# Kernel optimization log

Measured on AMD Instinct MI355X. Metric: run time of the kernel, lower is better.

Reference implementation:

```python
import jax, jax.numpy as jnp
import numpy as np

N = 100000      # nodes
E = 1600000     # edges (avg degree 16)
K = 3           # num_stacks
T = 4           # num_layers
H = 16          # hidden channels (conv1 out)
C = 1           # num_classes
BN_EPS = 1e-5


def setup_inputs() -> dict:
    key = jax.random.key(0)
    ks = jax.random.split(key, 14)
    s = 0.1
    return {
        "x": jax.random.normal(ks[0], (N, 1), jnp.float32),
        "edge_index": jax.random.randint(ks[1], (2, E), 0, N, dtype=jnp.int64),
        "edge_weight": jax.random.uniform(ks[2], (E,), jnp.float32),
        # conv1 (ARMAConv 1->16, K stacks, shared weights)
        "w1_init": jax.random.normal(ks[3], (K, 1, H), jnp.float32) * s,
        "w1_w":    jax.random.normal(ks[4], (K, H, H), jnp.float32) * s,
        "w1_root": jax.random.normal(ks[5], (K, 1, H), jnp.float32) * s,
        "w1_b":    jax.random.normal(ks[6], (K, H), jnp.float32) * s,
        "bn1_g": jnp.ones((H,), jnp.float32),
        "bn1_b": jnp.zeros((H,), jnp.float32),
        # conv2 (ARMAConv 16->1, act=None)
        "w2_init": jax.random.normal(ks[7], (K, H, C), jnp.float32) * s,
        "w2_w":    jax.random.normal(ks[8], (K, C, C), jnp.float32) * s,
        "w2_root": jax.random.normal(ks[9], (K, H, C), jnp.float32) * s,
        "w2_b":    jax.random.normal(ks[10], (K, C), jnp.float32) * s,
        # end linear 1->1
        "lin_w": jax.random.normal(ks[11], (C, C), jnp.float32) * s,
        "lin_b": jnp.zeros((C,), jnp.float32),
    }


def _arma_conv(x, src, dst, norm, init_w, w, root_w, bias, act):
    """PyG ARMAConv with shared weights. x: [N,Fin] -> [N,Fout]."""
    n = x.shape[0]
    # root/skip term (dropout is identity in eval); bias broadcast per stack
    root = jnp.einsum('ni,kio->nko', x, root_w) + bias[None, :, :]  # [N,K,Fout]
    out = jnp.einsum('ni,kio->nko', x, init_w)                      # t=0 transform
    for t in range(T):
        if t > 0:
            out = jnp.einsum('nki,kio->nko', out, w)                # shared weight
        msg = out[src] * norm[:, None, None]                        # [E,K,Fout]
        out = jax.ops.segment_sum(msg, dst, num_segments=n)         # A_hat @ out
        out = out + root
        if act:
            out = jax.nn.relu(out)
    return out.mean(axis=1)  # average over stacks


def reference(x, edge_index, edge_weight, w1_init, w1_w, w1_root, w1_b,
              bn1_g, bn1_b, w2_init, w2_w, w2_root, w2_b, lin_w, lin_b):
    src, dst = edge_index[0], edge_index[1]
    n = x.shape[0]
    # gcn_norm without self loops
    deg = jax.ops.segment_sum(edge_weight, dst, num_segments=n)
    dis = jnp.where(deg > 0, 1.0 / jnp.sqrt(deg), 0.0)
    norm = dis[src] * edge_weight * dis[dst]

    h = _arma_conv(x, src, dst, norm, w1_init, w1_w, w1_root, w1_b, act=True)
    # BatchNorm1d over node dim (batch statistics, deterministic)
    mu = h.mean(axis=0)
    var = h.var(axis=0)
    h = (h - mu) / jnp.sqrt(var + BN_EPS) * bn1_g + bn1_b
    h = jax.nn.relu(h)
    # dropout is identity in eval
    h = _arma_conv(h, src, dst, norm, w2_init, w2_w, w2_root, w2_b, act=False)
    h = h @ lin_w.T + lin_b
    return jax.nn.sigmoid(h)
```

## Files before the change

### kernel.cpp

```cpp
#include <hip/hip_runtime.h>
#include <hip/hip_bf16.h>
#include <math.h>


__global__ void zero_kernel(float* p, int n) {
    int i = blockIdx.x * blockDim.x + threadIdx.x;
    if (i < n) p[i] = 0.f;
}

__global__ void rank_kernel(const int* __restrict__ ei, int* __restrict__ cnt,
                            int* __restrict__ rank, int E) {
    int i = blockIdx.x * blockDim.x + threadIdx.x;
    if (i >= E) return;
    int dst = ei[E + i];
    rank[i] = atomicAdd(&cnt[dst], 1);
}

__global__ void scan1(const int* cnt, int* row_ptr, int* blockSums, int n) {
    __shared__ int sh[1024];
    int i = blockIdx.x * 1024 + threadIdx.x;
    int v = (i < n) ? cnt[i] : 0;
    sh[threadIdx.x] = v;
    __syncthreads();
    for (int off = 1; off < 1024; off <<= 1) {
        int t = 0;
        if (threadIdx.x >= off) t = sh[threadIdx.x - off];
        __syncthreads();
        sh[threadIdx.x] += t;
        __syncthreads();
    }
    if (i < n) row_ptr[i] = sh[threadIdx.x] - v;
    if (threadIdx.x == 1023) blockSums[blockIdx.x] = sh[1023];
}

__global__ void scan2(int* blockSums, int nb) {
    if (threadIdx.x == 0 && blockIdx.x == 0) {
        int run = 0;
        for (int i = 0; i < nb; i++) { int v = blockSums[i]; blockSums[i] = run; run += v; }
    }
}

__global__ void scan3(int* row_ptr, const int* blockSums, int n, int E) {
    int i = blockIdx.x * 1024 + threadIdx.x;
    if (i < n) row_ptr[i] += blockSums[blockIdx.x];
    if (i == 0) row_ptr[n] = E;
}

__global__ void place2(const int* __restrict__ ei, const float* __restrict__ ew,
                       const int* __restrict__ rank, const int* __restrict__ row_ptr,
                       int2* __restrict__ csr, int E) {
    int i = blockIdx.x * blockDim.x + threadIdx.x;
    if (i >= E) return;
    int s = ei[i];
    int d = ei[E + i];
    int pos = row_ptr[d] + rank[i];
    csr[pos] = make_int2(s, __float_as_int(ew[i]));
}

__global__ void wdeg_dis(const int2* __restrict__ csr, const int* __restrict__ row_ptr,
                         float* __restrict__ dis, int n) {
    int node = blockIdx.x * blockDim.x + threadIdx.x;
    if (node >= n) return;
    int p = row_ptr[node], end = row_ptr[node + 1];
    float s = 0.f;
    for (; p < end; p++) s += __int_as_float(csr[p].y);
    dis[node] = (s > 0.f) ? (1.0f / sqrtf(s)) : 0.f;
}

__global__ void normk(int2* __restrict__ csr, const int* __restrict__ row_ptr,
                      const float* __restrict__ dis, int n) {
    int node = blockIdx.x * blockDim.x + threadIdx.x;
    if (node >= n) return;
    int p = row_ptr[node], end = row_ptr[node + 1];
    float dn = dis[node];
    for (; p < end; p++) {
        int2 e = csr[p];
        csr[p].y = __float_as_int(__int_as_float(e.y) * dn * dis[e.x]);
    }
}


__global__ void aggx(const float* __restrict__ x, const int* __restrict__ row_ptr,
                     const int2* __restrict__ csr, float* __restrict__ y, int n) {
    int node = blockIdx.x * blockDim.x + threadIdx.x;
    if (node >= n) return;
    int p = row_ptr[node], end = row_ptr[node + 1];
    float a0 = 0.f, a1 = 0.f, a2 = 0.f, a3 = 0.f, a4 = 0.f, a5 = 0.f, a6 = 0.f, a7 = 0.f;
    for (; p + 7 < end; p += 8) {
        int2 e0 = csr[p], e1 = csr[p+1], e2 = csr[p+2], e3 = csr[p+3];
        int2 e4 = csr[p+4], e5 = csr[p+5], e6 = csr[p+6], e7 = csr[p+7];
        a0 += x[e0.x] * __int_as_float(e0.y);
        a1 += x[e1.x] * __int_as_float(e1.y);
        a2 += x[e2.x] * __int_as_float(e2.y);
        a3 += x[e3.x] * __int_as_float(e3.y);
        a4 += x[e4.x] * __int_as_float(e4.y);
        a5 += x[e5.x] * __int_as_float(e5.y);
        a6 += x[e6.x] * __int_as_float(e6.y);
        a7 += x[e7.x] * __int_as_float(e7.y);
    }
    for (; p + 1 < end; p += 2) {
        int2 e0 = csr[p], e1 = csr[p+1];
        a0 += x[e0.x] * __int_as_float(e0.y);
        a1 += x[e1.x] * __int_as_float(e1.y);
    }
    if (p < end) { int2 e = csr[p]; a0 += x[e.x] * __int_as_float(e.y); }
    y[node] = ((a0 + a1) + (a2 + a3)) + ((a4 + a5) + (a6 + a7));
}

__global__ void init48(const float* __restrict__ x, const float* __restrict__ y,
                       const float* __restrict__ w_init, const float* __restrict__ w_root,
                       const float* __restrict__ w_b, __hip_bfloat16* __restrict__ P, int n) {
    unsigned t = blockIdx.x * blockDim.x + threadIdx.x;
    if (t >= (unsigned)n * 64u) return;
    unsigned node = t >> 6, c = t & 63;
    float v = 0.f;
    if (c < 48) v = fmaxf(y[node] * w_init[c] + x[node] * w_root[c] + w_b[c], 0.f);
    P[t] = __float2bfloat16(v);
}

__global__ void __launch_bounds__(256) agg48f(
    const __hip_bfloat16* __restrict__ P, const float* __restrict__ W,
    const float* __restrict__ x, const float* __restrict__ w_root,
    const float* __restrict__ w_b, const int* __restrict__ row_ptr,
    const int2* __restrict__ csr, __hip_bfloat16* __restrict__ Pout, int n) {
    int wid = (int)((blockIdx.x * blockDim.x + threadIdx.x) >> 6);
    int lane = threadIdx.x & 63;
    if (wid >= n) return;
    unsigned orow = (unsigned)wid * 64u;
    if (lane >= 48) { Pout[orow + lane] = __float2bfloat16(0.f); return; }
    int k = lane >> 4, o = lane & 15;
    float wv[16];
#pragma unroll
    for (int i = 0; i < 16; i++) wv[i] = W[k * 256 + i * 16 + o];

    int p = row_ptr[wid], end = row_ptr[wid + 1];
    float a0 = 0.f, a1 = 0.f, a2 = 0.f, a3 = 0.f, a4 = 0.f, a5 = 0.f, a6 = 0.f, a7 = 0.f;
    for (; p + 7 < end; p += 8) {
        int2 e0 = csr[p], e1 = csr[p+1], e2 = csr[p+2], e3 = csr[p+3];
        int2 e4 = csr[p+4], e5 = csr[p+5], e6 = csr[p+6], e7 = csr[p+7];
        float q0 = __bfloat162float(P[(unsigned)e0.x * 64u + lane]);
        float q1 = __bfloat162float(P[(unsigned)e1.x * 64u + lane]);
        float q2 = __bfloat162float(P[(unsigned)e2.x * 64u + lane]);
        float q3 = __bfloat162float(P[(unsigned)e3.x * 64u + lane]);
        float q4 = __bfloat162float(P[(unsigned)e4.x * 64u + lane]);
        float q5 = __bfloat162float(P[(unsigned)e5.x * 64u + lane]);
        float q6 = __bfloat162float(P[(unsigned)e6.x * 64u + lane]);
        float q7 = __bfloat162float(P[(unsigned)e7.x * 64u + lane]);
        a0 += q0 * __int_as_float(e0.y);
        a1 += q1 * __int_as_float(e1.y);
        a2 += q2 * __int_as_float(e2.y);
        a3 += q3 * __int_as_float(e3.y);
        a4 += q4 * __int_as_float(e4.y);
        a5 += q5 * __int_as_float(e5.y);
        a6 += q6 * __int_as_float(e6.y);
        a7 += q7 * __int_as_float(e7.y);
    }
    for (; p + 1 < end; p += 2) {
        int2 e0 = csr[p], e1 = csr[p+1];
        a0 += __bfloat162float(P[(unsigned)e0.x * 64u + lane]) * __int_as_float(e0.y);
        a1 += __bfloat162float(P[(unsigned)e1.x * 64u + lane]) * __int_as_float(e1.y);
    }
    if (p < end) {
        int2 e = csr[p];
        a0 += __bfloat162float(P[(unsigned)e.x * 64u + lane]) * __int_as_float(e.y);
    }
    float S = ((a0 + a1) + (a2 + a3)) + ((a4 + a5) + (a6 + a7));

    float acc = 0.f;
    int base = lane & 48;
#pragma unroll
    for (int i = 0; i < 16; i++) {
        float sv = __shfl(S, base + i, 64);
        acc += sv * wv[i];
    }
    float v = acc + x[wid] * w_root[lane] + w_b[lane];
    Pout[orow + lane] = __float2bfloat16(fmaxf(v, 0.f));
}


__global__ void bn_stats(const __hip_bfloat16* __restrict__ P, float* __restrict__ acc, int n) {
    int tid = threadIdx.x;
    int c = tid & 15;
    int rowSlot = (int)((blockIdx.x * blockDim.x + tid) >> 4);
    int rowStride = (int)((gridDim.x * blockDim.x) >> 4);
    float s1 = 0.f, s2 = 0.f;
    for (int r = rowSlot; r < n; r += rowStride) {
        const __hip_bfloat16* row = &P[(unsigned)r * 64u];
        float h = (__bfloat162float(row[c]) + __bfloat162float(row[16 + c]) +
                   __bfloat162float(row[32 + c])) * (1.f / 3.f);
        s1 += h;
        s2 += h * h;
    }
    __shared__ float sh[256];
    sh[tid] = s1; __syncthreads();
    for (int off = 128; off >= 16; off >>= 1) { if (tid < off) sh[tid] += sh[tid + off]; __syncthreads(); }
    if (tid < 16) atomicAdd(&acc[tid], sh[tid]);
    __syncthreads();
    sh[tid] = s2; __syncthreads();
    for (int off = 128; off >= 16; off >>= 1) { if (tid < off) sh[tid] += sh[tid + off]; __syncthreads(); }
    if (tid < 16) atomicAdd(&acc[16 + tid], sh[tid]);
}

__global__ void bn_final(const float* acc, const float* g, const float* b,
                         float* coef, int n) {
    int c = threadIdx.x;
    if (c >= 16) return;
    float mu = acc[c] / (float)n;
    float var = acc[16 + c] / (float)n - mu * mu;
    float sc = g[c] / sqrtf(var + 1e-5f);
    coef[c] = sc;
    coef[16 + c] = b[c] - mu * sc;
}


__global__ void cvec_prep(const float* __restrict__ w2w, const float* __restrict__ w2i,
                          const float* __restrict__ w2r, const float* __restrict__ w2b,
                          float* __restrict__ cvec) {
    int c = threadIdx.x;
    float wk0 = w2w[0], wk1 = w2w[1], wk2 = w2w[2];
    const float inv3 = 1.f / 3.f;
    if (c < 16) {
        float psi = 0.f, r3 = 0.f, r2 = 0.f, r1 = 0.f, r0 = 0.f;
        float wks[3] = {wk0, wk1, wk2};
#pragma unroll
        for (int k = 0; k < 3; k++) {
            float w = wks[k], w2_ = w * w, w3 = w2_ * w;
            psi += w3 * w2i[k * 16 + c];
            float rr = w2r[k * 16 + c];
            r3 += w3 * rr; r2 += w2_ * rr; r1 += w * rr; r0 += rr;
        }
        cvec[c] = psi * inv3;
        cvec[16 + c] = r3 * inv3;
        cvec[32 + c] = r2 * inv3;
        cvec[48 + c] = r1 * inv3;
        cvec[64 + c] = r0 * inv3;
    } else if (c == 16) {
        float b3 = 0.f, b2 = 0.f, b1 = 0.f, b0 = 0.f;
        float wks[3] = {wk0, wk1, wk2};
#pragma unroll
        for (int k = 0; k < 3; k++) {
            float w = wks[k], w2_ = w * w, w3 = w2_ * w;
            float b = w2b[k];
            b3 += w3 * b; b2 += w2_ * b; b1 += w * b; b0 += b;
        }
        cvec[80] = b3 * inv3; cvec[81] = b2 * inv3; cvec[82] = b1 * inv3; cvec[83] = b0 * inv3;
    }
}

__global__ void conv2_init(const __hip_bfloat16* __restrict__ P, const float* __restrict__ coef,
                           const float* __restrict__ cvec,
                           float* __restrict__ z, float4* __restrict__ R, int n) {
    unsigned node = blockIdx.x * blockDim.x + threadIdx.x;
    if (node >= (unsigned)n) return;
    const __hip_bfloat16* row = &P[node * 64u];
    float zz = 0.f, r3 = cvec[80], r2 = cvec[81], r1 = cvec[82], r0 = cvec[83];
#pragma unroll
    for (int c = 0; c < 16; c++) {
        float h = (__bfloat162float(row[c]) + __bfloat162float(row[16 + c]) +
                   __bfloat162float(row[32 + c])) * (1.f / 3.f);
        float hb = fmaxf(h * coef[c] + coef[16 + c], 0.f);
        zz += hb * cvec[c];
        r3 += hb * cvec[16 + c];
        r2 += hb * cvec[32 + c];
        r1 += hb * cvec[48 + c];
        r0 += hb * cvec[64 + c];
    }
    z[node] = zz;
    R[node] = make_float4(r3, r2, r1, r0);
}

template<int FINAL>
__global__ void horner(const float* __restrict__ zin, const float* __restrict__ R, int comp,
                       const int* __restrict__ row_ptr, const int2* __restrict__ csr,
                       float* __restrict__ zout, const float* __restrict__ lw,
                       const float* __restrict__ lb, int n) {
    int node = blockIdx.x * blockDim.x + threadIdx.x;
    if (node >= n) return;
    int p = row_ptr[node], end = row_ptr[node + 1];
    float a0 = 0.f, a1 = 0.f, a2 = 0.f, a3 = 0.f, a4 = 0.f, a5 = 0.f, a6 = 0.f, a7 = 0.f;
    for (; p + 7 < end; p += 8) {
        int2 e0 = csr[p], e1 = csr[p+1], e2 = csr[p+2], e3 = csr[p+3];
        int2 e4 = csr[p+4], e5 = csr[p+5], e6 = csr[p+6], e7 = csr[p+7];
        a0 += zin[e0.x] * __int_as_float(e0.y);
        a1 += zin[e1.x] * __int_as_float(e1.y);
        a2 += zin[e2.x] * __int_as_float(e2.y);
        a3 += zin[e3.x] * __int_as_float(e3.y);
        a4 += zin[e4.x] * __int_as_float(e4.y);
        a5 += zin[e5.x] * __int_as_float(e5.y);
        a6 += zin[e6.x] * __int_as_float(e6.y);
        a7 += zin[e7.x] * __int_as_float(e7.y);
    }
    for (; p + 1 < end; p += 2) {
        int2 e0 = csr[p], e1 = csr[p+1];
        a0 += zin[e0.x] * __int_as_float(e0.y);
        a1 += zin[e1.x] * __int_as_float(e1.y);
    }
    if (p < end) { int2 e = csr[p]; a0 += zin[e.x] * __int_as_float(e.y); }
    float v = ((a0 + a1) + (a2 + a3)) + ((a4 + a5) + (a6 + a7)) + R[(unsigned)node * 4u + comp];
    if (FINAL) {
        float t = v * lw[0] + lb[0];
        zout[node] = 1.f / (1.f + expf(-t));
    } else {
        zout[node] = v;
    }
}


extern "C" void kernel_launch(void* const* d_in, const int* in_sizes, int n_in,
                              void* d_out, int out_size, void* d_ws, size_t ws_size,
                              hipStream_t stream) {
    const float* x = (const float*)d_in[0];
    const int* ei = (const int*)d_in[1];
    const float* ew = (const float*)d_in[2];
    const float* w1_init = (const float*)d_in[3];
    const float* w1_w = (const float*)d_in[4];
    const float* w1_root = (const float*)d_in[5];
    const float* w1_b = (const float*)d_in[6];
    const float* bn1_g = (const float*)d_in[7];
    const float* bn1_b = (const float*)d_in[8];
    const float* w2_init = (const float*)d_in[9];
    const float* w2_w = (const float*)d_in[10];
    const float* w2_root = (const float*)d_in[11];
    const float* w2_b = (const float*)d_in[12];
    const float* lin_w = (const float*)d_in[13];
    const float* lin_b = (const float*)d_in[14];

    const int N = in_sizes[0];
    const int E = in_sizes[2];
    float* out = (float*)d_out;

    char* ws = (char*)d_ws;
    size_t off = 0;
    auto alloc = [&](size_t bytes) {
        void* p = ws + off;
        off += (bytes + 15) & ~(size_t)15;
        return p;
    };
    int*   cnt       = (int*)  alloc((size_t)N * 4);
    int*   row_ptr   = (int*)  alloc((size_t)(N + 1) * 4);
    int*   blockSums = (int*)  alloc(128 * 4);
    float* bn_acc    = (float*)alloc(32 * 4);
    float* bn_coef   = (float*)alloc(32 * 4);
    float* cvec      = (float*)alloc(96 * 4);
    float* dis       = (float*)alloc((size_t)N * 4);
    float* y1        = (float*)alloc((size_t)N * 4);
    float* zA        = (float*)alloc((size_t)N * 4);
    float* zB        = (float*)alloc((size_t)N * 4);
    float4* Rbuf     = (float4*)alloc((size_t)N * 16);
    int2*  csr       = (int2*) alloc((size_t)E * 8);
    __hip_bfloat16* bufP = (__hip_bfloat16*)alloc((size_t)N * 64 * 2);
    __hip_bfloat16* bufQ = (__hip_bfloat16*)alloc((size_t)N * 64 * 2);
    int* rank = (int*)bufP;
    (void)ws_size;

    const int BS = 256;
    int gE = (E + BS - 1) / BS;
    int gN = (N + BS - 1) / BS;

    zero_kernel<<<gN, BS, 0, stream>>>((float*)cnt, N);
    zero_kernel<<<1, 32, 0, stream>>>(bn_acc, 32);

    rank_kernel<<<gE, BS, 0, stream>>>(ei, cnt, rank, E);
    int nb = (N + 1023) / 1024;
    scan1<<<nb, 1024, 0, stream>>>(cnt, row_ptr, blockSums, N);
    scan2<<<1, 64, 0, stream>>>(blockSums, nb);
    scan3<<<nb, 1024, 0, stream>>>(row_ptr, blockSums, N, E);
    place2<<<gE, BS, 0, stream>>>(ei, ew, rank, row_ptr, csr, E);
    wdeg_dis<<<gN, BS, 0, stream>>>(csr, row_ptr, dis, N);
    normk<<<gN, BS, 0, stream>>>(csr, row_ptr, dis, N);

    aggx<<<gN, BS, 0, stream>>>(x, row_ptr, csr, y1, N);
    int g64 = (N * 64 + BS - 1) / BS;
    init48<<<g64, BS, 0, stream>>>(x, y1, w1_init, w1_root, w1_b, bufP, N);
    int gAgg = (N + 3) / 4;
    agg48f<<<gAgg, BS, 0, stream>>>(bufP, w1_w, x, w1_root, w1_b, row_ptr, csr, bufQ, N);
    agg48f<<<gAgg, BS, 0, stream>>>(bufQ, w1_w, x, w1_root, w1_b, row_ptr, csr, bufP, N);
    agg48f<<<gAgg, BS, 0, stream>>>(bufP, w1_w, x, w1_root, w1_b, row_ptr, csr, bufQ, N);

    bn_stats<<<512, 256, 0, stream>>>(bufQ, bn_acc, N);
    bn_final<<<1, 16, 0, stream>>>(bn_acc, bn1_g, bn1_b, bn_coef, N);

    cvec_prep<<<1, 64, 0, stream>>>(w2_w, w2_init, w2_root, w2_b, cvec);
    conv2_init<<<gN, BS, 0, stream>>>(bufQ, bn_coef, cvec, zA, Rbuf, N);
    horner<0><<<gN, BS, 0, stream>>>(zA, (const float*)Rbuf, 0, row_ptr, csr, zB, lin_w, lin_b, N);
    horner<0><<<gN, BS, 0, stream>>>(zB, (const float*)Rbuf, 1, row_ptr, csr, zA, lin_w, lin_b, N);
    horner<0><<<gN, BS, 0, stream>>>(zA, (const float*)Rbuf, 2, row_ptr, csr, zB, lin_w, lin_b, N);
    horner<1><<<gN, BS, 0, stream>>>(zB, (const float*)Rbuf, 3, row_ptr, csr, out, lin_w, lin_b, N);
}
```

Before: 446.1 us.

## Split wave into half-waves gathering packed bf16 pairs; use nontemporal edge loads

The 48-channel aggregation kernel now has each half of a wavefront handle alternate edges, with each lane loading two packed bf16 channels as one 32-bit word. The two halves are combined by a cross-half shuffle, and the output is repacked through shuffles so 32 lanes write 4-byte words. This is meant to halve per-edge load instructions and widen each gather access. Separately, streaming edge-index and CSR reads across several kernels now use nontemporal loads to reduce cache pollution, at the cost of more shuffle and packing work per node.

New measurement: 544.8 us. 22.1% more time.

```diff
diff --git a/kernel.cpp b/kernel.cpp
--- a/kernel.cpp
+++ b/kernel.cpp
@@ -12,7 +12,7 @@
                             int* __restrict__ rank, int E) {
     int i = blockIdx.x * blockDim.x + threadIdx.x;
     if (i >= E) return;
-    int dst = ei[E + i];
+    int dst = __builtin_nontemporal_load(ei + E + i);
     rank[i] = atomicAdd(&cnt[dst], 1);
 }
 
@@ -51,8 +51,8 @@
                        int2* __restrict__ csr, int E) {
     int i = blockIdx.x * blockDim.x + threadIdx.x;
     if (i >= E) return;
-    int s = ei[i];
-    int d = ei[E + i];
+    int s = __builtin_nontemporal_load(ei + i);
+    int d = __builtin_nontemporal_load(ei + E + i);
     int pos = row_ptr[d] + rank[i];
     csr[pos] = make_int2(s, __float_as_int(ew[i]));
 }
@@ -84,26 +84,31 @@
                      const int2* __restrict__ csr, float* __restrict__ y, int n) {
     int node = blockIdx.x * blockDim.x + threadIdx.x;
     if (node >= n) return;
+    const long long* csr8 = (const long long*)csr;
     int p = row_ptr[node], end = row_ptr[node + 1];
     float a0 = 0.f, a1 = 0.f, a2 = 0.f, a3 = 0.f, a4 = 0.f, a5 = 0.f, a6 = 0.f, a7 = 0.f;
     for (; p + 7 < end; p += 8) {
-        int2 e0 = csr[p], e1 = csr[p+1], e2 = csr[p+2], e3 = csr[p+3];
-        int2 e4 = csr[p+4], e5 = csr[p+5], e6 = csr[p+6], e7 = csr[p+7];
-        a0 += x[e0.x] * __int_as_float(e0.y);
-        a1 += x[e1.x] * __int_as_float(e1.y);
-        a2 += x[e2.x] * __int_as_float(e2.y);
-        a3 += x[e3.x] * __int_as_float(e3.y);
-        a4 += x[e4.x] * __int_as_float(e4.y);
-        a5 += x[e5.x] * __int_as_float(e5.y);
-        a6 += x[e6.x] * __int_as_float(e6.y);
-        a7 += x[e7.x] * __int_as_float(e7.y);
-    }
-    for (; p + 1 < end; p += 2) {
-        int2 e0 = csr[p], e1 = csr[p+1];
-        a0 += x[e0.x] * __int_as_float(e0.y);
-        a1 += x[e1.x] * __int_as_float(e1.y);
-    }
-    if (p < end) { int2 e = csr[p]; a0 += x[e.x] * __int_as_float(e.y); }
+        long long e0 = __builtin_nontemporal_load(csr8 + p + 0);
+        long long e1 = __builtin_nontemporal_load(csr8 + p + 1);
+        long long e2 = __builtin_nontemporal_load(csr8 + p + 2);
+        long long e3 = __builtin_nontemporal_load(csr8 + p + 3);
+        long long e4 = __builtin_nontemporal_load(csr8 + p + 4);
+        long long e5 = __builtin_nontemporal_load(csr8 + p + 5);
+        long long e6 = __builtin_nontemporal_load(csr8 + p + 6);
+        long long e7 = __builtin_nontemporal_load(csr8 + p + 7);
+        a0 += x[(int)e0] * __int_as_float((int)(e0 >> 32));
+        a1 += x[(int)e1] * __int_as_float((int)(e1 >> 32));
+        a2 += x[(int)e2] * __int_as_float((int)(e2 >> 32));
+        a3 += x[(int)e3] * __int_as_float((int)(e3 >> 32));
+        a4 += x[(int)e4] * __int_as_float((int)(e4 >> 32));
+        a5 += x[(int)e5] * __int_as_float((int)(e5 >> 32));
+        a6 += x[(int)e6] * __int_as_float((int)(e6 >> 32));
+        a7 += x[(int)e7] * __int_as_float((int)(e7 >> 32));
+    }
+    for (; p < end; p++) {
+        long long e = __builtin_nontemporal_load(csr8 + p);
+        a0 += x[(int)e] * __int_as_float((int)(e >> 32));
+    }
     y[node] = ((a0 + a1) + (a2 + a3)) + ((a4 + a5) + (a6 + a7));
 }
 
@@ -118,7 +123,7 @@
     P[t] = __float2bfloat16(v);
 }
 
-__global__ void __launch_bounds__(256) agg48f(
+__global__ void __launch_bounds__(256) agg48p(
     const __hip_bfloat16* __restrict__ P, const float* __restrict__ W,
     const float* __restrict__ x, const float* __restrict__ w_root,
     const float* __restrict__ w_b, const int* __restrict__ row_ptr,
@@ -126,55 +131,82 @@
     int wid = (int)((blockIdx.x * blockDim.x + threadIdx.x) >> 6);
     int lane = threadIdx.x & 63;
     if (wid >= n) return;
-    unsigned orow = (unsigned)wid * 64u;
-    if (lane >= 48) { Pout[orow + lane] = __float2bfloat16(0.f); return; }
-    int k = lane >> 4, o = lane & 15;
+    int h = lane >> 5;
+    unsigned loff = (unsigned)((lane & 31) << 2);
+    const char* Pb = (const char*)P;
+    const long long* csr8 = (const long long*)csr;
+
+    int start = row_ptr[wid], end = row_ptr[wid + 1];
+    int p = start;
+    float l0 = 0.f, l1 = 0.f, l2 = 0.f, l3 = 0.f;
+    float h0 = 0.f, h1 = 0.f, h2 = 0.f, h3 = 0.f;
+    for (; p + 8 <= end; p += 8) {
+        long long e0 = __builtin_nontemporal_load(csr8 + p + 0 + h);
+        long long e1 = __builtin_nontemporal_load(csr8 + p + 2 + h);
+        long long e2 = __builtin_nontemporal_load(csr8 + p + 4 + h);
+        long long e3 = __builtin_nontemporal_load(csr8 + p + 6 + h);
+        unsigned o0 = (((unsigned)(int)e0) << 7) + loff;
+        unsigned o1 = (((unsigned)(int)e1) << 7) + loff;
+        unsigned o2 = (((unsigned)(int)e2) << 7) + loff;
+        unsigned o3 = (((unsigned)(int)e3) << 7) + loff;
+        unsigned u0 = *(const unsigned*)(Pb + o0);
+        unsigned u1 = *(const unsigned*)(Pb + o1);
+        unsigned u2 = *(const unsigned*)(Pb + o2);
+        unsigned u3 = *(const unsigned*)(Pb + o3);
+        float w0 = __int_as_float((int)(e0 >> 32));
+        float w1 = __int_as_float((int)(e1 >> 32));
+        float w2 = __int_as_float((int)(e2 >> 32));
+        float w3 = __int_as_float((int)(e3 >> 32));
+        l0 += __int_as_float(u0 << 16) * w0;
+        h0 += __int_as_float(u0 & 0xffff0000u) * w0;
+        l1 += __int_as_float(u1 << 16) * w1;
+        h1 += __int_as_float(u1 & 0xffff0000u) * w1;
+        l2 += __int_as_float(u2 << 16) * w2;
+        h2 += __int_as_float(u2 & 0xffff0000u) * w2;
+        l3 += __int_as_float(u3 << 16) * w3;
+        h3 += __int_as_float(u3 & 0xffff0000u) * w3;
+    }
+    for (; p < end; p += 2) {
+        int idx = p + h;
+        bool valid = idx < end;
+        long long e = __builtin_nontemporal_load(csr8 + (valid ? idx : p));
+        float w = valid ? __int_as_float((int)(e >> 32)) : 0.f;
+        unsigned o = (((unsigned)(int)e) << 7) + loff;
+        unsigned u = *(const unsigned*)(Pb + o);
+        l0 += __int_as_float(u << 16) * w;
+        h0 += __int_as_float(u & 0xffff0000u) * w;
+    }
+    float Slo = (l0 + l1) + (l2 + l3);
+    float Shi = (h0 + h1) + (h2 + h3);
+    Slo += __shfl_xor(Slo, 32);
+    Shi += __shfl_xor(Shi, 32);
+
+    int c = lane;
+    int k = c >> 4;
+    int kk = (k < 3) ? k : 0;
     float wv[16];
 #pragma unroll
-    for (int i = 0; i < 16; i++) wv[i] = W[k * 256 + i * 16 + o];
-
-    int p = row_ptr[wid], end = row_ptr[wid + 1];
-    float a0 = 0.f, a1 = 0.f, a2 = 0.f, a3 = 0.f, a4 = 0.f, a5 = 0.f, a6 = 0.f, a7 = 0.f;
-    for (; p + 7 < end; p += 8) {
-        int2 e0 = csr[p], e1 = csr[p+1], e2 = csr[p+2], e3 = csr[p+3];
-        int2 e4 = csr[p+4], e5 = csr[p+5], e6 = csr[p+6], e7 = csr[p+7];
-        float q0 = __bfloat162float(P[(unsigned)e0.x * 64u + lane]);
-        float q1 = __bfloat162float(P[(unsigned)e1.x * 64u + lane]);
-        float q2 = __bfloat162float(P[(unsigned)e2.x * 64u + lane]);
-        float q3 = __bfloat162float(P[(unsigned)e3.x * 64u + lane]);
-        float q4 = __bfloat162float(P[(unsigned)e4.x * 64u + lane]);
-        float q5 = __bfloat162float(P[(unsigned)e5.x * 64u + lane]);
-        float q6 = __bfloat162float(P[(unsigned)e6.x * 64u + lane]);
-        float q7 = __bfloat162float(P[(unsigned)e7.x * 64u + lane]);
-        a0 += q0 * __int_as_float(e0.y);
-        a1 += q1 * __int_as_float(e1.y);
-        a2 += q2 * __int_as_float(e2.y);
-        a3 += q3 * __int_as_float(e3.y);
-        a4 += q4 * __int_as_float(e4.y);
-        a5 += q5 * __int_as_float(e5.y);
-        a6 += q6 * __int_as_float(e6.y);
-        a7 += q7 * __int_as_float(e7.y);
-    }
-    for (; p + 1 < end; p += 2) {
-        int2 e0 = csr[p], e1 = csr[p+1];
-        a0 += __bfloat162float(P[(unsigned)e0.x * 64u + lane]) * __int_as_float(e0.y);
-        a1 += __bfloat162float(P[(unsigned)e1.x * 64u + lane]) * __int_as_float(e1.y);
-    }
-    if (p < end) {
-        int2 e = csr[p];
-        a0 += __bfloat162float(P[(unsigned)e.x * 64u + lane]) * __int_as_float(e.y);
-    }
-    float S = ((a0 + a1) + (a2 + a3)) + ((a4 + a5) + (a6 + a7));
-
+    for (int i = 0; i < 16; i++) wv[i] = W[kk * 256 + i * 16 + (c & 15)];
+    float rootc = 0.f;
+    if (c < 48) rootc = x[wid] * w_root[c] + w_b[c];
     float acc = 0.f;
-    int base = lane & 48;
+    int bl = kk << 3;
 #pragma unroll
-    for (int i = 0; i < 16; i++) {
-        float sv = __shfl(S, base + i, 64);
-        acc += sv * wv[i];
-    }
-    float v = acc + x[wid] * w_root[lane] + w_b[lane];
-    Pout[orow + lane] = __float2bfloat16(fmaxf(v, 0.f));
+    for (int i2 = 0; i2 < 8; i2++) {
+        acc += __shfl(Slo, bl + i2) * wv[2 * i2];
+        acc += __shfl(Shi, bl + i2) * wv[2 * i2 + 1];
+    }
+    float r = (c < 48) ? fmaxf(acc + rootc, 0.f) : 0.f;
+
+    __hip_bfloat16 hb = __float2bfloat16(r);
+    unsigned bu = (unsigned)*reinterpret_cast<unsigned short*>(&hb);
+    int j2 = (lane & 31) << 1;
+    unsigned lo = (unsigned)__shfl((int)bu, j2);
+    unsigned hi = (unsigned)__shfl((int)bu, j2 + 1);
+    if (lane < 32) {
+        unsigned d = (lo & 0xffffu) | (hi << 16);
+        *(unsigned*)((char*)Pout + (((unsigned)wid) << 7) + loff) = d;
+    }
 }
 
 
@@ -276,26 +308,31 @@
                        const float* __restrict__ lb, int n) {
     int node = blockIdx.x * blockDim.x + threadIdx.x;
     if (node >= n) return;
+    const long long* csr8 = (const long long*)csr;
     int p = row_ptr[node], end = row_ptr[node + 1];
     float a0 = 0.f, a1 = 0.f, a2 = 0.f, a3 = 0.f, a4 = 0.f, a5 = 0.f, a6 = 0.f, a7 = 0.f;
     for (; p + 7 < end; p += 8) {
-        int2 e0 = csr[p], e1 = csr[p+1], e2 = csr[p+2], e3 = csr[p+3];
-        int2 e4 = csr[p+4], e5 = csr[p+5], e6 = csr[p+6], e7 = csr[p+7];
-        a0 += zin[e0.x] * __int_as_float(e0.y);
-        a1 += zin[e1.x] * __int_as_float(e1.y);
-        a2 += zin[e2.x] * __int_as_float(e2.y);
-        a3 += zin[e3.x] * __int_as_float(e3.y);
-        a4 += zin[e4.x] * __int_as_float(e4.y);
-        a5 += zin[e5.x] * __int_as_float(e5.y);
-        a6 += zin[e6.x] * __int_as_float(e6.y);
-        a7 += zin[e7.x] * __int_as_float(e7.y);
-    }
-    for (; p + 1 < end; p += 2) {
-        int2 e0 = csr[p], e1 = csr[p+1];
-        a0 += zin[e0.x] * __int_as_float(e0.y);
-        a1 += zin[e1.x] * __int_as_float(e1.y);
-    }
-    if (p < end) { int2 e = csr[p]; a0 += zin[e.x] * __int_as_float(e.y); }
+        long long e0 = __builtin_nontemporal_load(csr8 + p + 0);
+        long long e1 = __builtin_nontemporal_load(csr8 + p + 1);
+        long long e2 = __builtin_nontemporal_load(csr8 + p + 2);
+        long long e3 = __builtin_nontemporal_load(csr8 + p + 3);
+        long long e4 = __builtin_nontemporal_load(csr8 + p + 4);
+        long long e5 = __builtin_nontemporal_load(csr8 + p + 5);
+        long long e6 = __builtin_nontemporal_load(csr8 + p + 6);
+        long long e7 = __builtin_nontemporal_load(csr8 + p + 7);
+        a0 += zin[(int)e0] * __int_as_float((int)(e0 >> 32));
+        a1 += zin[(int)e1] * __int_as_float((int)(e1 >> 32));
+        a2 += zin[(int)e2] * __int_as_float((int)(e2 >> 32));
+        a3 += zin[(int)e3] * __int_as_float((int)(e3 >> 32));
+        a4 += zin[(int)e4] * __int_as_float((int)(e4 >> 32));
+        a5 += zin[(int)e5] * __int_as_float((int)(e5 >> 32));
+        a6 += zin[(int)e6] * __int_as_float((int)(e6 >> 32));
+        a7 += zin[(int)e7] * __int_as_float((int)(e7 >> 32));
+    }
+    for (; p < end; p++) {
+        long long e = __builtin_nontemporal_load(csr8 + p);
+        a0 += zin[(int)e] * __int_as_float((int)(e >> 32));
+    }
     float v = ((a0 + a1) + (a2 + a3)) + ((a4 + a5) + (a6 + a7)) + R[(unsigned)node * 4u + comp];
     if (FINAL) {
         float t = v * lw[0] + lb[0];
@@ -373,9 +410,9 @@
     int g64 = (N * 64 + BS - 1) / BS;
     init48<<<g64, BS, 0, stream>>>(x, y1, w1_init, w1_root, w1_b, bufP, N);
     int gAgg = (N + 3) / 4;
-    agg48f<<<gAgg, BS, 0, stream>>>(bufP, w1_w, x, w1_root, w1_b, row_ptr, csr, bufQ, N);
-    agg48f<<<gAgg, BS, 0, stream>>>(bufQ, w1_w, x, w1_root, w1_b, row_ptr, csr, bufP, N);
-    agg48f<<<gAgg, BS, 0, stream>>>(bufP, w1_w, x, w1_root, w1_b, row_ptr, csr, bufQ, N);
+    agg48p<<<gAgg, BS, 0, stream>>>(bufP, w1_w, x, w1_root, w1_b, row_ptr, csr, bufQ, N);
+    agg48p<<<gAgg, BS, 0, stream>>>(bufQ, w1_w, x, w1_root, w1_b, row_ptr, csr, bufP, N);
+    agg48p<<<gAgg, BS, 0, stream>>>(bufP, w1_w, x, w1_root, w1_b, row_ptr, csr, bufQ, N);
 
     bn_stats<<<512, 256, 0, stream>>>(bufQ, bn_acc, N);
     bn_final<<<1, 16, 0, stream>>>(bn_acc, bn1_g, bn1_b, bn_coef, N);
```
